# Kernel optimization log

Hardware: AMD Instinct MI355X
Metric: run time of the kernel (lower is better)

## Reference

```python
import jax, jax.numpy as jnp
import numpy as np

B, L, C = 4, 2048, 1024

def setup_inputs() -> dict:
    key = jax.random.key(0)
    k1, k2, k3 = jax.random.split(key, 3)
    net_in = jax.random.normal(k1, (B, L, C), dtype=jnp.float32)
    # torch Linear weights stored as (out, in); we keep that convention
    w_qkv = jax.random.normal(k2, (3 * C, C), dtype=jnp.float32) * (1.0 / np.sqrt(C))
    w_out = jax.random.normal(k3, (C, C), dtype=jnp.float32) * (1.0 / np.sqrt(C))
    return {"net_in": net_in, "w_qkv": w_qkv, "w_out": w_out}

def reference(net_in, w_qkv, w_out):
    Bc, Lc, Cc = net_in.shape
    qkv = jnp.einsum('blc,dc->bld', net_in, w_qkv)  # (B, L, 3C)
    q, k, v = jnp.split(qkv, 3, axis=-1)
    attn = jnp.einsum('bqc,bkc->bqk', q, k) / jnp.sqrt(jnp.float32(Cc))
    causal = jnp.tril(jnp.ones((Lc, Lc), dtype=bool))
    attn = jnp.where(causal[None, :, :], attn, -jnp.inf)
    attn = jax.nn.softmax(attn, axis=-1)
    out = jnp.einsum('bqk,bkc->bqc', attn, v)
    return jnp.einsum('blc,dc->bld', out, w_out)
```

## Files before the change

kernel.cpp:

```cpp
#include <hip/hip_runtime.h>
#include <hip/hip_bf16.h>
#include <cstdint>
#include <cstddef>

typedef __hip_bfloat16 bf16;
typedef float  floatx4 __attribute__((ext_vector_type(4)));
typedef __bf16 bf16x8  __attribute__((ext_vector_type(8)));

typedef __attribute__((address_space(1))) void as1_void;
typedef __attribute__((address_space(3))) void as3_void;

constexpr int Bn = 4, Ln = 2048, Cn = 1024;

__device__ __forceinline__ void store_one(float* p, float v) { *p = v; }
__device__ __forceinline__ void store_one(bf16*  p, float v) { *p = __float2bfloat16(v); }

#define BAR()    asm volatile("s_barrier" ::: "memory")
#define VMCNT2() asm volatile("s_waitcnt vmcnt(2)" ::: "memory")
#define VMCNT0() asm volatile("s_waitcnt vmcnt(0)" ::: "memory")
#define SCHEDB() __builtin_amdgcn_sched_barrier(0)
#define STAGE(gp, off) \
    __builtin_amdgcn_global_load_lds((const as1_void*)(gp), (as3_void*)(smem + (off)), 16, 0, 0)

__device__ __forceinline__ void gemm256_core(
    char* __restrict__ smem,
    const bf16* __restrict__ A, const bf16* __restrict__ B,
    int m0, int n0, int kbeg, int kend, int lda, int ldb,
    floatx4 (&acc)[8][4])
{
    const int tid  = threadIdx.x;
    const int lane = tid & 63;
    const int quad = lane >> 4;
    const int lr   = lane & 15;
    const int wave = tid >> 6;
    const int wm   = (wave >> 2) * 128;
    const int wn   = (wave & 3) * 64;

#pragma unroll
    for (int i = 0; i < 8; ++i)
#pragma unroll
        for (int j = 0; j < 4; ++j) { floatx4 z = {0.f, 0.f, 0.f, 0.f}; acc[i][j] = z; }

    const int srow = tid >> 3;
    const int sx   = (tid & 7) ^ (srow & 7);
    const bf16* gA = A + (size_t)(m0 + srow) * lda + sx * 8 + kbeg;
    const bf16* gB = B + (size_t)(n0 + srow) * ldb + sx * 8 + kbeg;
    const int wuni = __builtin_amdgcn_readfirstlane((tid & 0x1C0) * 16);

    const int aoff = (wm + lr) * 64;
    const int boff = (wn + lr) * 64;
    const int s0   = (quad ^ (lr & 7)) * 8;

    const int NT = (kend - kbeg) >> 6;

    STAGE(gB,             32768 + 0 * 8192 + wuni);
    STAGE(gB + 64  * ldb, 32768 + 1 * 8192 + wuni);
    STAGE(gB + 128 * ldb, 32768 + 2 * 8192 + wuni);
    STAGE(gB + 192 * ldb, 32768 + 3 * 8192 + wuni);
    STAGE(gA,                     0 * 8192 + wuni);
    STAGE(gA + 128 * lda,         2 * 8192 + wuni);
    STAGE(gA + 64  * lda,         1 * 8192 + wuni);
    STAGE(gA + 192 * lda,         3 * 8192 + wuni);
    VMCNT2();
    BAR();

#define LDA4(MB, SK) do { _Pragma("unroll") for (int ii = 0; ii < 4; ++ii) \
        a[ii] = *(const bf16x8*)(As + aoff + ((MB) * 4 + ii) * 1024 + (SK)); } while (0)
#define LDB4(SK) do { _Pragma("unroll") for (int nn = 0; nn < 4; ++nn) \
        b[nn] = *(const bf16x8*)(Bs + boff + nn * 1024 + (SK)); } while (0)
#define MFMA16(MB) do { _Pragma("unroll") for (int ii = 0; ii < 4; ++ii) { \
        _Pragma("unroll") for (int nn = 0; nn < 4; ++nn) \
            acc[(MB) * 4 + ii][nn] = __builtin_amdgcn_mfma_f32_16x16x32_bf16( \
                a[ii], b[nn], acc[(MB) * 4 + ii][nn], 0, 0, 0); } } while (0)

    for (int t = 0; t < NT; ++t) {
        const bf16* As = (const bf16*)(smem + (t & 1) * 65536);
        const bf16* Bs = (const bf16*)(smem + (t & 1) * 65536 + 32768);
        const int  wl  = ((t + 1) & 1) * 65536;
        const int  kn  = (t + 1) << 6;
        const bool more = (t + 1 < NT);
        bf16x8 a[4], b[4];

        LDB4(s0);
        LDA4(0, s0);
        if (more) {
            STAGE(gB + kn,            wl + 32768 + 0 * 8192 + wuni);
            STAGE(gB + kn + 64 * ldb, wl + 32768 + 1 * 8192 + wuni);
        }
        BAR(); SCHEDB();
        __builtin_amdgcn_s_setprio(1);
        MFMA16(0);
        __builtin_amdgcn_s_setprio(0);
        SCHEDB();
        if (more) VMCNT2(); else VMCNT0();
        BAR();

        LDA4(1, s0);
        if (more) {
            STAGE(gB + kn + 128 * ldb, wl + 32768 + 2 * 8192 + wuni);
            STAGE(gB + kn + 192 * ldb, wl + 32768 + 3 * 8192 + wuni);
        }
        BAR(); SCHEDB();
        __builtin_amdgcn_s_setprio(1);
        MFMA16(1);
        __builtin_amdgcn_s_setprio(0);
        SCHEDB();
        BAR();

        LDB4(s0 ^ 32);
        LDA4(0, s0 ^ 32);
        if (more) {
            STAGE(gA + kn,             wl + 0 * 8192 + wuni);
            STAGE(gA + kn + 128 * lda, wl + 2 * 8192 + wuni);
        }
        BAR(); SCHEDB();
        __builtin_amdgcn_s_setprio(1);
        MFMA16(0);
        __builtin_amdgcn_s_setprio(0);
        SCHEDB();
        BAR();

        LDA4(1, s0 ^ 32);
        if (more) {
            STAGE(gA + kn + 64  * lda, wl + 1 * 8192 + wuni);
            STAGE(gA + kn + 192 * lda, wl + 3 * 8192 + wuni);
        }
        BAR(); SCHEDB();
        __builtin_amdgcn_s_setprio(1);
        MFMA16(1);
        __builtin_amdgcn_s_setprio(0);
        SCHEDB();
        if (more) VMCNT2();
        BAR();
    }
#undef LDA4
#undef LDB4
#undef MFMA16
}

template <typename OutT>
__device__ __forceinline__ void gemm256(
    char* __restrict__ smem,
    const bf16* __restrict__ A, const bf16* __restrict__ B, OutT* __restrict__ C,
    int m0, int n0, int kbeg, int kend, int lda, int ldb, int ldc, float cscale)
{
    floatx4 acc[8][4];
    gemm256_core(smem, A, B, m0, n0, kbeg, kend, lda, ldb, acc);

    const int lane = threadIdx.x & 63;
    const int quad = lane >> 4;
    const int lr   = lane & 15;
    const int wave = threadIdx.x >> 6;
    const int wm   = (wave >> 2) * 128;
    const int wn   = (wave & 3) * 64;

#pragma unroll
    for (int mi = 0; mi < 8; ++mi) {
        const int row = m0 + wm + mi * 16 + quad * 4;
#pragma unroll
        for (int n = 0; n < 4; ++n) {
            const int col = n0 + wn + n * 16 + lr;
            OutT* cp = C + (size_t)row * ldc + col;
#pragma unroll
            for (int r = 0; r < 4; ++r)
                store_one(cp + (size_t)r * ldc, acc[mi][n][r] * cscale);
        }
    }
}

__device__ __forceinline__ void gemm_m128n256(
    char* __restrict__ smem,
    const bf16* __restrict__ A, const bf16* __restrict__ B, bf16* __restrict__ C,
    int m0, int n0, int kend, int lda, int ldb, int ldc)
{
    const int tid  = threadIdx.x;
    const int lane = tid & 63;
    const int quad = lane >> 4;
    const int lr   = lane & 15;
    const int wave = tid >> 6;
    const int wm   = (wave >> 2) * 64;
    const int wn   = (wave & 3) * 64;

    floatx4 acc[4][4];
#pragma unroll
    for (int i = 0; i < 4; ++i)
#pragma unroll
        for (int j = 0; j < 4; ++j) { floatx4 z = {0.f, 0.f, 0.f, 0.f}; acc[i][j] = z; }

    const int srow = tid >> 3;
    const int sx   = (tid & 7) ^ (srow & 7);
    const bf16* gA = A + (size_t)(m0 + srow) * lda + sx * 8;
    const bf16* gB = B + (size_t)(n0 + srow) * ldb + sx * 8;
    const int wuni = __builtin_amdgcn_readfirstlane((tid & 0x1C0) * 16);

    const int aoff = (wm + lr) * 64;
    const int boff = (wn + lr) * 64;
    const int s0   = (quad ^ (lr & 7)) * 8;

    const int NT  = kend >> 6;
    const int BUF = 49152;

    STAGE(gA,             0 * 8192 + wuni);
    STAGE(gA + 64 * lda,  1 * 8192 + wuni);
    STAGE(gB,             16384 + 0 * 8192 + wuni);
    STAGE(gB + 64  * ldb, 16384 + 1 * 8192 + wuni);
    STAGE(gB + 128 * ldb, 16384 + 2 * 8192 + wuni);
    STAGE(gB + 192 * ldb, 16384 + 3 * 8192 + wuni);
    VMCNT0();
    BAR();

#define LDA2(PH, SK) do { _Pragma("unroll") for (int ii = 0; ii < 2; ++ii) \
        a[ii] = *(const bf16x8*)(As + aoff + ((PH) * 2 + ii) * 1024 + (SK)); } while (0)
#define LDB4(SK) do { _Pragma("unroll") for (int nn = 0; nn < 4; ++nn) \
        b[nn] = *(const bf16x8*)(Bs + boff + nn * 1024 + (SK)); } while (0)
#define MFMA8(PH) do { _Pragma("unroll") for (int ii = 0; ii < 2; ++ii) { \
        _Pragma("unroll") for (int nn = 0; nn < 4; ++nn) \
            acc[(PH) * 2 + ii][nn] = __builtin_amdgcn_mfma_f32_16x16x32_bf16( \
                a[ii], b[nn], acc[(PH) * 2 + ii][nn], 0, 0, 0); } } while (0)

    for (int t = 0; t < NT; ++t) {
        const bf16* As = (const bf16*)(smem + (t & 1) * BUF);
        const bf16* Bs = (const bf16*)(smem + (t & 1) * BUF + 16384);
        const int  wl  = ((t + 1) & 1) * BUF;
        const int  kn  = (t + 1) << 6;
        const bool more = (t + 1 < NT);
        bf16x8 a[2], b[4];

        LDB4(s0);
        LDA2(0, s0);
        if (more) {
            STAGE(gB + kn,            wl + 16384 + 0 * 8192 + wuni);
            STAGE(gB + kn + 64 * ldb, wl + 16384 + 1 * 8192 + wuni);
        }
        BAR(); SCHEDB();
        __builtin_amdgcn_s_setprio(1);
        MFMA8(0);
        __builtin_amdgcn_s_setprio(0);
        SCHEDB();
        BAR();

        LDA2(1, s0);
        if (more) {
            STAGE(gB + kn + 128 * ldb, wl + 16384 + 2 * 8192 + wuni);
            STAGE(gB + kn + 192 * ldb, wl + 16384 + 3 * 8192 + wuni);
        }
        BAR(); SCHEDB();
        __builtin_amdgcn_s_setprio(1);
        MFMA8(1);
        __builtin_amdgcn_s_setprio(0);
        SCHEDB();
        BAR();

        LDB4(s0 ^ 32);
        LDA2(0, s0 ^ 32);
        if (more) {
            STAGE(gA + kn,            wl + 0 * 8192 + wuni);
            STAGE(gA + kn + 64 * lda, wl + 1 * 8192 + wuni);
        }
        BAR(); SCHEDB();
        __builtin_amdgcn_s_setprio(1);
        MFMA8(0);
        __builtin_amdgcn_s_setprio(0);
        SCHEDB();
        BAR();

        LDA2(1, s0 ^ 32);
        BAR(); SCHEDB();
        __builtin_amdgcn_s_setprio(1);
        MFMA8(1);
        __builtin_amdgcn_s_setprio(0);
        SCHEDB();
        if (more) VMCNT0();
        BAR();
    }
#undef LDA2
#undef LDB4
#undef MFMA8

#pragma unroll
    for (int mi = 0; mi < 4; ++mi) {
        const int row = m0 + wm + mi * 16 + quad * 4;
#pragma unroll
        for (int n = 0; n < 4; ++n) {
            const int col = n0 + wn + n * 16 + lr;
            bf16* cp = C + (size_t)row * ldc + col;
#pragma unroll
            for (int r = 0; r < 4; ++r)
                store_one(cp + (size_t)r * ldc, acc[mi][n][r]);
        }
    }
}

__device__ __forceinline__ void gemm_m128n128(
    char* __restrict__ smem,
    const bf16* __restrict__ A, const bf16* __restrict__ B, float* __restrict__ C,
    int m0, int n0, int kend, int lda, int ldb, int ldc)
{
    const int tid  = threadIdx.x;
    const int lane = tid & 63;
    const int quad = lane >> 4;
    const int lr   = lane & 15;
    const int wave = tid >> 6;
    const int wm   = (wave >> 2) * 64;
    const int wn   = (wave & 3) * 32;

    floatx4 acc[4][2];
#pragma unroll
    for (int i = 0; i < 4; ++i)
#pragma unroll
        for (int j = 0; j < 2; ++j) { floatx4 z = {0.f, 0.f, 0.f, 0.f}; acc[i][j] = z; }

    const int srow = tid >> 3;
    const int sx   = (tid & 7) ^ (srow & 7);
    const bf16* gA = A + (size_t)(m0 + srow) * lda + sx * 8;
    const bf16* gB = B + (size_t)(n0 + srow) * ldb + sx * 8;
    const int wuni = __builtin_amdgcn_readfirstlane((tid & 0x1C0) * 16);

    const int aoff = (wm + lr) * 64;
    const int boff = (wn + lr) * 64;
    const int s0   = (quad ^ (lr & 7)) * 8;

    const int NT  = kend >> 6;
    const int BUF = 32768;

    STAGE(gA,            0 * 8192 + wuni);
    STAGE(gA + 64 * lda, 1 * 8192 + wuni);
    STAGE(gB,            16384 + 0 * 8192 + wuni);
    STAGE(gB + 64 * ldb, 16384 + 1 * 8192 + wuni);
    VMCNT0();
    BAR();

#define LDA2(PH, SK) do { _Pragma("unroll") for (int ii = 0; ii < 2; ++ii) \
        a[ii] = *(const bf16x8*)(As + aoff + ((PH) * 2 + ii) * 1024 + (SK)); } while (0)
#define LDB2(SK) do { _Pragma("unroll") for (int nn = 0; nn < 2; ++nn) \
        b[nn] = *(const bf16x8*)(Bs + boff + nn * 1024 + (SK)); } while (0)
#define MFMA4(PH) do { _Pragma("unroll") for (int ii = 0; ii < 2; ++ii) { \
        _Pragma("unroll") for (int nn = 0; nn < 2; ++nn) \
            acc[(PH) * 2 + ii][nn] = __builtin_amdgcn_mfma_f32_16x16x32_bf16( \
                a[ii], b[nn], acc[(PH) * 2 + ii][nn], 0, 0, 0); } } while (0)

    for (int t = 0; t < NT; ++t) {
        const bf16* As = (const bf16*)(smem + (t & 1) * BUF);
        const bf16* Bs = (const bf16*)(smem + (t & 1) * BUF + 16384);
        const int  wl  = ((t + 1) & 1) * BUF;
        const int  kn  = (t + 1) << 6;
        const bool more = (t + 1 < NT);
        bf16x8 a[2], b[2];

        LDB2(s0);
        LDA2(0, s0);
        if (more) {
            STAGE(gB + kn,            wl + 16384 + 0 * 8192 + wuni);
            STAGE(gB + kn + 64 * ldb, wl + 16384 + 1 * 8192 + wuni);
        }
        BAR(); SCHEDB();
        __builtin_amdgcn_s_setprio(1);
        MFMA4(0);
        __builtin_amdgcn_s_setprio(0);
        SCHEDB();
        BAR();

        LDA2(1, s0);
        if (more) {
            STAGE(gA + kn,            wl + 0 * 8192 + wuni);
            STAGE(gA + kn + 64 * lda, wl + 1 * 8192 + wuni);
        }
        BAR(); SCHEDB();
        __builtin_amdgcn_s_setprio(1);
        MFMA4(1);
        __builtin_amdgcn_s_setprio(0);
        SCHEDB();
        BAR();

        LDB2(s0 ^ 32);
        LDA2(0, s0 ^ 32);
        BAR(); SCHEDB();
        __builtin_amdgcn_s_setprio(1);
        MFMA4(0);
        __builtin_amdgcn_s_setprio(0);
        SCHEDB();
        BAR();

        LDA2(1, s0 ^ 32);
        BAR(); SCHEDB();
        __builtin_amdgcn_s_setprio(1);
        MFMA4(1);
        __builtin_amdgcn_s_setprio(0);
        SCHEDB();
        if (more) VMCNT0();
        BAR();
    }
#undef LDA2
#undef LDB2
#undef MFMA4

#pragma unroll
    for (int mi = 0; mi < 4; ++mi) {
        const int row = m0 + wm + mi * 16 + quad * 4;
#pragma unroll
        for (int n = 0; n < 2; ++n) {
            const int col = n0 + wn + n * 16 + lr;
            float* cp = C + (size_t)row * ldc + col;
#pragma unroll
            for (int r = 0; r < 4; ++r)
                cp[(size_t)r * ldc] = acc[mi][n][r];
        }
    }
}

__global__ __launch_bounds__(512, 2)
void g1_qk(const bf16* __restrict__ Xb, const bf16* __restrict__ Wqkb,
           bf16* __restrict__ QK)
{
    __shared__ __align__(16) char smem[131072];
    const int i = blockIdx.x;
    const int j = i >> 3;
    const int mt = (i & 7) * 4 + (j & 3);
    const int nt = j >> 2;
    gemm256<bf16>(smem, Xb, Wqkb, QK, mt * 256, nt * 256, 0, 1024, 1024, 1024, 2048, 1.0f);
}

__global__ __launch_bounds__(512, 2)
void g2_s_w2(const bf16* __restrict__ QK, const bf16* __restrict__ Wob,
             const bf16* __restrict__ WvT, bf16* __restrict__ S,
             bf16* __restrict__ W2)
{
    __shared__ __align__(16) char smem[131072];
    const int i = blockIdx.x;
    if (i < 144) {
        const int b = (i & 7) >> 1;
        const int t = (i >> 3) * 2 + (i & 1);
        int ti = (int)((sqrtf(8.f * t + 1.f) - 1.f) * 0.5f);
        while ((ti + 1) * (ti + 2) / 2 <= t) ++ti;
        while (ti * (ti + 1) / 2 > t) --ti;
        const int tj = t - ti * (ti + 1) / 2;
        const bf16* Aq = QK + (size_t)b * Ln * 2048;
        const bf16* Bk = Aq + 1024;
        bf16* Sb = S + (size_t)b * Ln * Ln;
        gemm256<bf16>(smem, Aq, Bk, Sb, ti * 256, tj * 256, 0, 1024, 2048, 2048, Ln, 0.03125f);
    } else {
        const int j = i - 144;
        gemm256<bf16>(smem, Wob, WvT, W2, (j & 3) * 256, (j >> 2) * 256, 0, 1024, 1024, 1024, 1024, 1.0f);
    }
}

__device__ __forceinline__ float waveMax(float x) {
#pragma unroll
    for (int o = 32; o > 0; o >>= 1) x = fmaxf(x, __shfl_xor(x, o, 64));
    return x;
}
__device__ __forceinline__ float waveSum(float x) {
#pragma unroll
    for (int o = 32; o > 0; o >>= 1) x += __shfl_xor(x, o, 64);
    return x;
}

__device__ void softmax_rows32(bf16* __restrict__ S, int row0)
{
    const int wave = threadIdx.x >> 6, lane = threadIdx.x & 63;
    for (int it4 = 0; it4 < 4; ++it4) {
        const int row = row0 + wave * 4 + it4;
        const int q = row & (Ln - 1);
        bf16* Srow = S + (size_t)row * Ln;
        const int kmax = ((q >> 7) + 1) << 7;
        const int nv = (kmax + 511) >> 9;
        float x[4][8];
        float m = -1e30f;
        for (int it = 0; it < nv; ++it) {
            int c0 = it * 512 + lane * 8;
            bf16x8 v = *(const bf16x8*)(Srow + c0);
#pragma unroll
            for (int e = 0; e < 8; ++e) {
                float f = (float)v[e];
                f = (c0 + e <= q) ? f : -1e30f;
                x[it][e] = f;
                m = fmaxf(m, f);
            }
        }
        m = waveMax(m);
        float s = 0.f;
        for (int it = 0; it < nv; ++it)
#pragma unroll
            for (int e = 0; e < 8; ++e) {
                float ex = (x[it][e] > -1e29f) ? __expf(x[it][e] - m) : 0.f;
                x[it][e] = ex;
                s += ex;
            }
        s = waveSum(s);
        const float inv = 1.f / s;
        for (int it = 0; it < nv; ++it) {
            bf16x8 o;
#pragma unroll
            for (int e = 0; e < 8; ++e) o[e] = (__bf16)(x[it][e] * inv);
            *(bf16x8*)(Srow + it * 512 + lane * 8) = o;
        }
    }
}

__global__ __launch_bounds__(512, 2)
void g3_vwt_sm(const bf16* __restrict__ W2, const bf16* __restrict__ Xb,
               bf16* __restrict__ VWT, bf16* __restrict__ S)
{
    __shared__ __align__(16) char smem[98304];
    const int i = blockIdx.x;
    const int j = i >> 3;
    const int nt = (i & 7) * 4 + (j & 3);
    const int mh = j >> 2;
    gemm_m128n256(smem, W2, Xb, VWT, mh * 128, nt * 256, 1024, 1024, 1024, 8192);
    softmax_rows32(S, i * 32);
}

__global__ __launch_bounds__(512, 2)
void g4_out(const bf16* __restrict__ P, const bf16* __restrict__ VWT,
            float* __restrict__ out)
{
    __shared__ __align__(16) char smem[65536];
    const int i = blockIdx.x;
    const int r = i & 7;
    const int b = r >> 1, p = r & 1;
    const int q = i >> 3;
    const int nt = p * 4 + (q & 3);
    const int mh = q >> 2;

    const bf16* Pp = P + (size_t)b * Ln * Ln;
    const bf16* Bv = VWT + (size_t)b * Ln;
    float* Co = out + (size_t)b * Ln * Cn;
    const int n0 = nt * 128;

    gemm_m128n128(smem, Pp, Bv, Co, (15 - mh) * 128, n0, (16 - mh) * 128, Ln, 8192, Cn);
    gemm_m128n128(smem, Pp, Bv, Co, mh * 128,        n0, (mh + 1) * 128,  Ln, 8192, Cn);
}

__global__ __launch_bounds__(256)
void cast_all(const float* __restrict__ X, const float* __restrict__ Wqkv,
              const float* __restrict__ Wo,
              bf16* __restrict__ Xb, bf16* __restrict__ Wqkb,
              bf16* __restrict__ Wob, bf16* __restrict__ WvT)
{
    int blk = blockIdx.x;
    if (blk < 11264) {
        int i = blk * 256 + threadIdx.x;
        const float* src; bf16* dst; int off;
        if (i < 2097152)                 { src = X;    dst = Xb;   off = i; }
        else if (i < 2097152 + 524288)   { src = Wqkv; dst = Wqkb; off = i - 2097152; }
        else                             { src = Wo;   dst = Wob;  off = i - 2621440; }
        float4 f = ((const float4*)src)[off];
        bf16 o0 = __float2bfloat16(f.x), o1 = __float2bfloat16(f.y);
        bf16 o2 = __float2bfloat16(f.z), o3 = __float2bfloat16(f.w);
        ushort4 u;
        u.x = *(unsigned short*)&o0; u.y = *(unsigned short*)&o1;
        u.z = *(unsigned short*)&o2; u.w = *(unsigned short*)&o3;
        *(ushort4*)(dst + (size_t)off * 4) = u;
    } else {
        __shared__ float t[32][33];
        int tt = blk - 11264;
        int c0 = (tt & 31) * 32;
        int r0 = (tt >> 5) * 32;
        const float* Wv = Wqkv + 2048 * 1024;
        int xcol = threadIdx.x & 31, y0 = threadIdx.x >> 5;
#pragma unroll
        for (int p = 0; p < 4; ++p) {
            int y = y0 + 8 * p;
            t[y][xcol] = Wv[(size_t)(r0 + y) * 1024 + c0 + xcol];
        }
        __syncthreads();
#pragma unroll
        for (int p = 0; p < 4; ++p) {
            int mloc = y0 + 8 * p;
            WvT[(size_t)(c0 + mloc) * 1024 + r0 + xcol] = __float2bfloat16(t[xcol][mloc]);
        }
    }
}

extern "C" void kernel_launch(void* const* d_in, const int* in_sizes, int n_in,
                              void* d_out, int out_size, void* d_ws, size_t ws_size,
                              hipStream_t stream)
{
    const float* X    = (const float*)d_in[0];
    const float* Wqkv = (const float*)d_in[1];
    const float* Wout = (const float*)d_in[2];
    float* out = (float*)d_out;

    char* ws = (char*)d_ws;
    const size_t MiB = 1024ull * 1024ull;
    bf16* Xb   = (bf16*)(ws + 0);
    bf16* QK   = (bf16*)(ws + 16 * MiB);
    bf16* VWT  = (bf16*)(ws + 48 * MiB);
    bf16* Sbuf = (bf16*)(ws + 64 * MiB);
    bf16* Wqkb = (bf16*)(ws + 96 * MiB);
    bf16* WvT  = (bf16*)(ws + 100 * MiB);
    bf16* Wob  = (bf16*)(ws + 102 * MiB);
    bf16* W2   = (bf16*)(ws + 104 * MiB);

    cast_all<<<dim3(12288), 256, 0, stream>>>(X, Wqkv, Wout, Xb, Wqkb, Wob, WvT);

    g1_qk<<<dim3(256), 512, 0, stream>>>(Xb, Wqkb, QK);

    g2_s_w2<<<dim3(160), 512, 0, stream>>>(QK, Wob, WvT, Sbuf, W2);

    g3_vwt_sm<<<dim3(256), 512, 0, stream>>>(W2, Xb, VWT, Sbuf);

    g4_out<<<dim3(256), 512, 0, stream>>>(Sbuf, VWT, out);
}
```

Before: 224.1 us.

## Triple-buffer LDS staging in GEMM cores and stride softmax rows across blocks

Converts the double-buffered global-to-LDS pipelines in the m128n256 and m128n128 GEMM cores to a three-stage ring. Each iteration now prefetches two tiles ahead and waits with partial vmcnt counts rather than draining all loads, so memory latency is hidden deeper. In exchange the shared memory footprint grows to 144KB and 96KB per block, which can cut occupancy below the two blocks per CU that the launch bounds request. Separately, softmax rows are now strided across blocks instead of taken as contiguous chunks, which spreads the causal row lengths evenly across blocks.

After: 225.1 us. About the same (+0.4%).

```diff
diff --git a/kernel.cpp b/kernel.cpp
--- a/kernel.cpp
+++ b/kernel.cpp
@@ -17,6 +17,8 @@
 
 #define BAR()    asm volatile("s_barrier" ::: "memory")
 #define VMCNT2() asm volatile("s_waitcnt vmcnt(2)" ::: "memory")
+#define VMCNT4() asm volatile("s_waitcnt vmcnt(4)" ::: "memory")
+#define VMCNT6() asm volatile("s_waitcnt vmcnt(6)" ::: "memory")
 #define VMCNT0() asm volatile("s_waitcnt vmcnt(0)" ::: "memory")
 #define SCHEDB() __builtin_amdgcn_sched_barrier(0)
 #define STAGE(gp, off) \
@@ -200,13 +202,16 @@
     const int NT  = kend >> 6;
     const int BUF = 49152;
 
-    STAGE(gA,             0 * 8192 + wuni);
-    STAGE(gA + 64 * lda,  1 * 8192 + wuni);
-    STAGE(gB,             16384 + 0 * 8192 + wuni);
-    STAGE(gB + 64  * ldb, 16384 + 1 * 8192 + wuni);
-    STAGE(gB + 128 * ldb, 16384 + 2 * 8192 + wuni);
-    STAGE(gB + 192 * ldb, 16384 + 3 * 8192 + wuni);
-    VMCNT0();
+#define STG_B01(KN, bo) do { STAGE(gB + (KN),            (bo) + 16384 + 0 * 8192 + wuni); \
+                             STAGE(gB + (KN) + 64 * ldb, (bo) + 16384 + 1 * 8192 + wuni); } while (0)
+#define STG_B23(KN, bo) do { STAGE(gB + (KN) + 128 * ldb, (bo) + 16384 + 2 * 8192 + wuni); \
+                             STAGE(gB + (KN) + 192 * ldb, (bo) + 16384 + 3 * 8192 + wuni); } while (0)
+#define STG_A01(KN, bo) do { STAGE(gA + (KN),            (bo) + 0 * 8192 + wuni); \
+                             STAGE(gA + (KN) + 64 * lda, (bo) + 1 * 8192 + wuni); } while (0)
+
+    STG_B01(0, 0); STG_B23(0, 0); STG_A01(0, 0);
+    if (NT > 1) { STG_B01(64, BUF); STG_B23(64, BUF); STG_A01(64, BUF); VMCNT6(); }
+    else        { VMCNT0(); }
     BAR();
 
 #define LDA2(PH, SK) do { _Pragma("unroll") for (int ii = 0; ii < 2; ++ii) \
@@ -218,20 +223,20 @@
             acc[(PH) * 2 + ii][nn] = __builtin_amdgcn_mfma_f32_16x16x32_bf16( \
                 a[ii], b[nn], acc[(PH) * 2 + ii][nn], 0, 0, 0); } } while (0)
 
+    int cur = 0;
     for (int t = 0; t < NT; ++t) {
-        const bf16* As = (const bf16*)(smem + (t & 1) * BUF);
-        const bf16* Bs = (const bf16*)(smem + (t & 1) * BUF + 16384);
-        const int  wl  = ((t + 1) & 1) * BUF;
-        const int  kn  = (t + 1) << 6;
-        const bool more = (t + 1 < NT);
+        const bf16* As = (const bf16*)(smem + cur * BUF);
+        const bf16* Bs = (const bf16*)(smem + cur * BUF + 16384);
+        const int  st  = (cur >= 1) ? cur - 1 : 2;
+        const int  wl  = st * BUF;
+        const int  kn  = (t + 2) << 6;
+        const bool more1 = (t + 1 < NT);
+        const bool more2 = (t + 2 < NT);
         bf16x8 a[2], b[4];
 
         LDB4(s0);
         LDA2(0, s0);
-        if (more) {
-            STAGE(gB + kn,            wl + 16384 + 0 * 8192 + wuni);
-            STAGE(gB + kn + 64 * ldb, wl + 16384 + 1 * 8192 + wuni);
-        }
+        if (more2) STG_B01(kn, wl);
         BAR(); SCHEDB();
         __builtin_amdgcn_s_setprio(1);
         MFMA8(0);
@@ -240,10 +245,7 @@
         BAR();
 
         LDA2(1, s0);
-        if (more) {
-            STAGE(gB + kn + 128 * ldb, wl + 16384 + 2 * 8192 + wuni);
-            STAGE(gB + kn + 192 * ldb, wl + 16384 + 3 * 8192 + wuni);
-        }
+        if (more2) STG_B23(kn, wl);
         BAR(); SCHEDB();
         __builtin_amdgcn_s_setprio(1);
         MFMA8(1);
@@ -253,10 +255,7 @@
 
         LDB4(s0 ^ 32);
         LDA2(0, s0 ^ 32);
-        if (more) {
-            STAGE(gA + kn,            wl + 0 * 8192 + wuni);
-            STAGE(gA + kn + 64 * lda, wl + 1 * 8192 + wuni);
-        }
+        if (more2) STG_A01(kn, wl);
         BAR(); SCHEDB();
         __builtin_amdgcn_s_setprio(1);
         MFMA8(0);
@@ -270,12 +269,17 @@
         MFMA8(1);
         __builtin_amdgcn_s_setprio(0);
         SCHEDB();
-        if (more) VMCNT0();
-        BAR();
+        if (more2)      VMCNT6();
+        else if (more1) VMCNT0();
+        BAR();
+        cur = (cur == 2) ? 0 : cur + 1;
     }
 #undef LDA2
 #undef LDB4
 #undef MFMA8
+#undef STG_B01
+#undef STG_B23
+#undef STG_A01
 
 #pragma unroll
     for (int mi = 0; mi < 4; ++mi) {
@@ -323,11 +327,14 @@
     const int NT  = kend >> 6;
     const int BUF = 32768;
 
-    STAGE(gA,            0 * 8192 + wuni);
-    STAGE(gA + 64 * lda, 1 * 8192 + wuni);
-    STAGE(gB,            16384 + 0 * 8192 + wuni);
-    STAGE(gB + 64 * ldb, 16384 + 1 * 8192 + wuni);
-    VMCNT0();
+#define STG_B01(KN, bo) do { STAGE(gB + (KN),            (bo) + 16384 + 0 * 8192 + wuni); \
+                             STAGE(gB + (KN) + 64 * ldb, (bo) + 16384 + 1 * 8192 + wuni); } while (0)
+#define STG_A01(KN, bo) do { STAGE(gA + (KN),            (bo) + 0 * 8192 + wuni); \
+                             STAGE(gA + (KN) + 64 * lda, (bo) + 1 * 8192 + wuni); } while (0)
+
+    STG_B01(0, 0); STG_A01(0, 0);
+    if (NT > 1) { STG_B01(64, BUF); STG_A01(64, BUF); VMCNT4(); }
+    else        { VMCNT0(); }
     BAR();
 
 #define LDA2(PH, SK) do { _Pragma("unroll") for (int ii = 0; ii < 2; ++ii) \
@@ -339,20 +346,20 @@
             acc[(PH) * 2 + ii][nn] = __builtin_amdgcn_mfma_f32_16x16x32_bf16( \
                 a[ii], b[nn], acc[(PH) * 2 + ii][nn], 0, 0, 0); } } while (0)
 
+    int cur = 0;
     for (int t = 0; t < NT; ++t) {
-        const bf16* As = (const bf16*)(smem + (t & 1) * BUF);
-        const bf16* Bs = (const bf16*)(smem + (t & 1) * BUF + 16384);
-        const int  wl  = ((t + 1) & 1) * BUF;
-        const int  kn  = (t + 1) << 6;
-        const bool more = (t + 1 < NT);
+        const bf16* As = (const bf16*)(smem + cur * BUF);
+        const bf16* Bs = (const bf16*)(smem + cur * BUF + 16384);
+        const int  st  = (cur >= 1) ? cur - 1 : 2;
+        const int  wl  = st * BUF;
+        const int  kn  = (t + 2) << 6;
+        const bool more1 = (t + 1 < NT);
+        const bool more2 = (t + 2 < NT);
         bf16x8 a[2], b[2];
 
         LDB2(s0);
         LDA2(0, s0);
-        if (more) {
-            STAGE(gB + kn,            wl + 16384 + 0 * 8192 + wuni);
-            STAGE(gB + kn + 64 * ldb, wl + 16384 + 1 * 8192 + wuni);
-        }
+        if (more2) STG_B01(kn, wl);
         BAR(); SCHEDB();
         __builtin_amdgcn_s_setprio(1);
         MFMA4(0);
@@ -361,10 +368,7 @@
         BAR();
 
         LDA2(1, s0);
-        if (more) {
-            STAGE(gA + kn,            wl + 0 * 8192 + wuni);
-            STAGE(gA + kn + 64 * lda, wl + 1 * 8192 + wuni);
-        }
+        if (more2) STG_A01(kn, wl);
         BAR(); SCHEDB();
         __builtin_amdgcn_s_setprio(1);
         MFMA4(1);
@@ -387,12 +391,16 @@
         MFMA4(1);
         __builtin_amdgcn_s_setprio(0);
         SCHEDB();
-        if (more) VMCNT0();
-        BAR();
+        if (more2)      VMCNT4();
+        else if (more1) VMCNT0();
+        BAR();
+        cur = (cur == 2) ? 0 : cur + 1;
     }
 #undef LDA2
 #undef LDB2
 #undef MFMA4
+#undef STG_B01
+#undef STG_A01
 
 #pragma unroll
     for (int mi = 0; mi < 4; ++mi) {
@@ -455,11 +463,11 @@
     return x;
 }
 
-__device__ void softmax_rows32(bf16* __restrict__ S, int row0)
+__device__ void softmax_rows_strided(bf16* __restrict__ S, int i)
 {
     const int wave = threadIdx.x >> 6, lane = threadIdx.x & 63;
     for (int it4 = 0; it4 < 4; ++it4) {
-        const int row = row0 + wave * 4 + it4;
+        const int row = i + 256 * (wave * 4 + it4);
         const int q = row & (Ln - 1);
         bf16* Srow = S + (size_t)row * Ln;
         const int kmax = ((q >> 7) + 1) << 7;
@@ -501,20 +509,20 @@
 void g3_vwt_sm(const bf16* __restrict__ W2, const bf16* __restrict__ Xb,
                bf16* __restrict__ VWT, bf16* __restrict__ S)
 {
-    __shared__ __align__(16) char smem[98304];
+    __shared__ __align__(16) char smem[147456];
     const int i = blockIdx.x;
     const int j = i >> 3;
     const int nt = (i & 7) * 4 + (j & 3);
     const int mh = j >> 2;
     gemm_m128n256(smem, W2, Xb, VWT, mh * 128, nt * 256, 1024, 1024, 1024, 8192);
-    softmax_rows32(S, i * 32);
+    softmax_rows_strided(S, i);
 }
 
 __global__ __launch_bounds__(512, 2)
 void g4_out(const bf16* __restrict__ P, const bf16* __restrict__ VWT,
             float* __restrict__ out)
 {
-    __shared__ __align__(16) char smem[65536];
+    __shared__ __align__(16) char smem[98304];
     const int i = blockIdx.x;
     const int r = i & 7;
     const int b = r >> 1, p = r & 1;
```
